# Performance work log

Hardware: AMD Instinct MI355X
Metric: run time of the kernel (lower is better)

## Reference

```python
import jax, jax.numpy as jnp
import numpy as np

B, T, C, H = 4, 4096, 1024, 128

def setup_inputs() -> dict:
    key = jax.random.key(0)
    kx, kq, kk, kv = jax.random.split(key, 4)
    s = 1.0 / np.sqrt(C)
    return {
        "x": jax.random.normal(kx, (B, T, C), dtype=jnp.float32),
        "Wq": jax.random.normal(kq, (C, H), dtype=jnp.float32) * s,
        "Wk": jax.random.normal(kk, (C, H), dtype=jnp.float32) * s,
        "Wv": jax.random.normal(kv, (C, H), dtype=jnp.float32) * s,
    }

def reference(x, Wq, Wk, Wv):
    # x: [B,T,C]; projections to [B,T,H]
    q = jnp.einsum('btc,ch->bth', x, Wq)
    k = jnp.einsum('btc,ch->bth', x, Wk)
    v = jnp.einsum('btc,ch->bth', x, Wv)
    scale = 1.0 / jnp.sqrt(jnp.asarray(H, dtype=x.dtype))
    wei = jnp.einsum('bqh,bkh->bqk', q, k) * scale  # [B,T,T]
    causal = jnp.tril(jnp.ones((T, T), dtype=bool))
    wei = jnp.where(causal, wei, -jnp.inf)
    wei = jax.nn.softmax(wei, axis=-1)
    # dropout p=0.0 -> identity
    out = jnp.einsum('bqk,bkh->bqh', wei, v)
    return out
```

## Files before the change

### kernel.cpp

```cpp
#include <hip/hip_runtime.h>
#include <hip/hip_bf16.h>

#define B_ 4
#define T_ 4096
#define C_ 1024
#define H_ 128
#define SEG_ 8

typedef __attribute__((ext_vector_type(8))) short short8;
typedef __attribute__((ext_vector_type(4))) float f32x4;
typedef __attribute__((ext_vector_type(4))) unsigned short u16x4;

static __device__ __forceinline__ unsigned short f2bf(float f) {
    union { float f; unsigned u; } v; v.f = f;
    unsigned r = v.u + 0x7FFF + ((v.u >> 16) & 1);
    return (unsigned short)(r >> 16);
}

__global__ void wt_kernel(const float* __restrict__ Wq, const float* __restrict__ Wk,
                          const float* __restrict__ Wv, unsigned short* __restrict__ Wt) {
    __shared__ float tile[64][65];
    int c0 = blockIdx.x * 64, h0 = blockIdx.y * 64, w = blockIdx.z;
    const float* W = (w == 0) ? Wq : (w == 1) ? Wk : Wv;
    unsigned short* dst = Wt + (size_t)w * H_ * C_;
    int tr = threadIdx.x >> 6, tc = threadIdx.x & 63;
#pragma unroll
    for (int p = 0; p < 16; ++p) {
        int r = p * 4 + tr;
        tile[r][tc] = W[(size_t)(c0 + r) * H_ + h0 + tc];
    }
    __syncthreads();
#pragma unroll
    for (int p = 0; p < 16; ++p) {
        int r = p * 4 + tr;
        dst[(size_t)(h0 + r) * C_ + c0 + tc] = f2bf(tile[tc][r]);
    }
}

__global__ __launch_bounds__(256) void proj_kernel(
        const float* __restrict__ x, const unsigned short* __restrict__ Wt3,
        unsigned short* __restrict__ Q, unsigned short* __restrict__ K,
        unsigned short* __restrict__ Vt) {
    __shared__ unsigned short Xs[32 * 64];
    int m0 = blockIdx.x * 32;
    int tid = threadIdx.x;
    int lane = tid & 63, wid = tid >> 6;
    int l15 = lane & 15, g = lane >> 4;
    int l7 = l15 & 7;

    f32x4 acc[2][6];
#pragma unroll
    for (int i = 0; i < 2; i++)
#pragma unroll
        for (int j = 0; j < 6; j++) acc[i][j] = (f32x4)0.0f;

    for (int kt = 0; kt < C_ / 64; ++kt) {
        int k0 = kt * 64;
        {
            int r = tid >> 3, c8 = tid & 7;
            const float* src = x + (size_t)(m0 + r) * C_ + k0 + c8 * 8;
            float4 v0 = *(const float4*)src;
            float4 v1 = *(const float4*)(src + 4);
            union { short8 s; u16x4 h[2]; } pk;
            pk.h[0].x = f2bf(v0.x); pk.h[0].y = f2bf(v0.y);
            pk.h[0].z = f2bf(v0.z); pk.h[0].w = f2bf(v0.w);
            pk.h[1].x = f2bf(v1.x); pk.h[1].y = f2bf(v1.y);
            pk.h[1].z = f2bf(v1.z); pk.h[1].w = f2bf(v1.w);
            *(short8*)&Xs[r * 64 + ((c8 ^ (r & 7)) << 3)] = pk.s;
        }
        __syncthreads();
#pragma unroll
        for (int kf = 0; kf < 2; ++kf) {
            short8 a[2], bv[6];
#pragma unroll
            for (int mt = 0; mt < 2; mt++) {
                int row = mt * 16 + l15;
                a[mt] = *(const short8*)&Xs[row * 64 + (((kf * 4 + g) ^ l7) << 3)];
            }
#pragma unroll
            for (int nt = 0; nt < 6; nt++) {
                int r = wid * 96 + nt * 16 + l15;
                bv[nt] = *(const short8*)(Wt3 + (size_t)r * C_ + k0 + (kf * 4 + g) * 8);
            }
#pragma unroll
            for (int mt = 0; mt < 2; mt++)
#pragma unroll
                for (int nt = 0; nt < 6; nt++)
                    acc[mt][nt] = __builtin_amdgcn_mfma_f32_16x16x32_bf16(a[mt], bv[nt], acc[mt][nt], 0, 0, 0);
        }
        __syncthreads();
    }
    int b = m0 >> 12;
    int tbase = m0 & (T_ - 1);
#pragma unroll
    for (int nt = 0; nt < 6; nt++) {
        int col = wid * 96 + nt * 16 + l15;
        int w = col >> 7, h = col & 127;
#pragma unroll
        for (int mt = 0; mt < 2; mt++) {
            if (w < 2) {
                unsigned short* outp = (w == 0) ? Q : K;
                int row0 = m0 + mt * 16 + g * 4;
#pragma unroll
                for (int ri = 0; ri < 4; ri++)
                    outp[(size_t)(row0 + ri) * H_ + h] = f2bf(acc[mt][nt][ri]);
            } else {
                int t0 = tbase + mt * 16 + g * 4;
                u16x4 o;
                o.x = f2bf(acc[mt][nt][0]); o.y = f2bf(acc[mt][nt][1]);
                o.z = f2bf(acc[mt][nt][2]); o.w = f2bf(acc[mt][nt][3]);
                *(u16x4*)&Vt[(size_t)(b * H_ + h) * T_ + t0] = o;
            }
        }
    }
}

__global__ __launch_bounds__(256) void attn_kernel(
        const unsigned short* __restrict__ Q, const unsigned short* __restrict__ K,
        const unsigned short* __restrict__ Vt,
        float* __restrict__ Opart, float* __restrict__ Lpart) {
    int qb = blockIdx.x, seg = blockIdx.y, b = blockIdx.z;
    if (seg * SEG_ > qb) return;
    __shared__ unsigned short KsF[64 * 128];
    __shared__ unsigned short VsF[128 * 64];
    __shared__ unsigned short PsF[4][16 * 64];
    int tid = threadIdx.x, lane = tid & 63, wid = tid >> 6;
    int l15 = lane & 15, g = lane >> 4;
    int l7 = l15 & 7;
    int q0w = qb * 64 + wid * 16;
    const float alpha = 0.08838834764831845f;

    short8 aq[4];
#pragma unroll
    for (int kf = 0; kf < 4; kf++)
        aq[kf] = *(const short8*)(Q + (size_t)(b * T_ + q0w + l15) * H_ + kf * 32 + g * 8);

    f32x4 o[8];
#pragma unroll
    for (int i = 0; i < 8; i++) o[i] = (f32x4)0.0f;
    float l_run[4];
#pragma unroll
    for (int ri = 0; ri < 4; ri++) l_run[ri] = 0.f;

    int kt0 = seg * SEG_;
    int kt_end = min(qb, kt0 + SEG_ - 1);

    short8 kreg[4], vreg[4];
#define LOAD_KV(KT) do { int k0_ = (KT) * 64; \
    _Pragma("unroll") \
    for (int p = 0; p < 4; ++p) { int idx = tid + p * 256; \
        kreg[p] = *(const short8*)(K + (size_t)(b * T_ + k0_ + (idx >> 4)) * H_ + (idx & 15) * 8); } \
    _Pragma("unroll") \
    for (int p = 0; p < 4; ++p) { int idx = tid + p * 256; \
        vreg[p] = *(const short8*)(Vt + (size_t)(b * H_ + (idx >> 3)) * T_ + k0_ + (idx & 7) * 8); } \
    } while (0)

    LOAD_KV(kt0);
    for (int kt = kt0; kt <= kt_end; ++kt) {
        int k0 = kt * 64;
        __syncthreads();
#pragma unroll
        for (int p = 0; p < 4; ++p) {
            int idx = tid + p * 256;
            int r = idx >> 4;
            *(short8*)&KsF[r * 128 + (((idx & 15) ^ (r & 7)) << 3)] = kreg[p];
        }
#pragma unroll
        for (int p = 0; p < 4; ++p) {
            int idx = tid + p * 256;
            int r = idx >> 3;
            *(short8*)&VsF[r * 64 + (((idx & 7) ^ (r & 7)) << 3)] = vreg[p];
        }
        __syncthreads();
        if (kt < kt_end) LOAD_KV(kt + 1);

        f32x4 s[4];
#pragma unroll
        for (int ct = 0; ct < 4; ct++) {
            s[ct] = (f32x4)0.0f;
#pragma unroll
            for (int kf = 0; kf < 4; kf++) {
                int row = ct * 16 + l15;
                short8 bk = *(const short8*)&KsF[row * 128 + (((kf * 4 + g) ^ l7) << 3)];
                s[ct] = __builtin_amdgcn_mfma_f32_16x16x32_bf16(aq[kf], bk, s[ct], 0, 0, 0);
            }
        }
        bool diag = (kt == qb);
#pragma unroll
        for (int ct = 0; ct < 4; ct++)
#pragma unroll
            for (int ri = 0; ri < 4; ri++) {
                float v = s[ct][ri] * alpha;
                if (diag) {
                    int kkg = k0 + ct * 16 + l15;
                    int qg = q0w + g * 4 + ri;
                    if (kkg > qg) v = -1e30f;
                }
                float p = __expf(v);
                l_run[ri] += p;
                int row = g * 4 + ri;
                PsF[wid][row * 64 + (((2 * ct + (l15 >> 3)) ^ (row & 7)) << 3) + l7] = f2bf(p);
            }

#pragma unroll
        for (int kf2 = 0; kf2 < 2; kf2++) {
            short8 ap = *(const short8*)&PsF[wid][l15 * 64 + (((kf2 * 4 + g) ^ l7) << 3)];
#pragma unroll
            for (int ht = 0; ht < 8; ht++) {
                int row = ht * 16 + l15;
                short8 bv = *(const short8*)&VsF[row * 64 + (((kf2 * 4 + g) ^ l7) << 3)];
                o[ht] = __builtin_amdgcn_mfma_f32_16x16x32_bf16(ap, bv, o[ht], 0, 0, 0);
            }
        }
    }
#undef LOAD_KV

    size_t slot = (((size_t)b * (T_ / 64) + qb) * 8 + seg);
    float* Ob = Opart + slot * 64 * 128;
    float* Lb = Lpart + slot * 64;
#pragma unroll
    for (int ri = 0; ri < 4; ri++) {
        float l = l_run[ri];
#pragma unroll
        for (int off = 1; off < 16; off <<= 1)
            l += __shfl_xor(l, off, 64);
        int qrow = wid * 16 + g * 4 + ri;
        Lb[qrow] = l;
#pragma unroll
        for (int ht = 0; ht < 8; ht++)
            Ob[(size_t)qrow * 128 + ht * 16 + l15] = o[ht][ri];
    }
}

__global__ __launch_bounds__(256) void combine_kernel(
        const float* __restrict__ Opart, const float* __restrict__ Lpart,
        float* __restrict__ out) {
    int qt = blockIdx.x, b = blockIdx.y;
    int nseg = qt / SEG_ + 1;
    int tid = threadIdx.x;
    size_t obase = (((size_t)b * (T_ / 64) + qt) * 8) * 64 * 128;
    size_t lbase = (((size_t)b * (T_ / 64) + qt) * 8) * 64;
    float4* dst = (float4*)(out + ((size_t)b * T_ + qt * 64) * 128);
#pragma unroll
    for (int i = 0; i < 8; ++i) {
        int e4 = tid + i * 256;
        int q = e4 >> 5;
        float4 acc = {0.f, 0.f, 0.f, 0.f};
        float lsum = 0.f;
        for (int s = 0; s < nseg; ++s) {
            float4 v = *((const float4*)(Opart + obase + (size_t)s * 64 * 128) + e4);
            acc.x += v.x; acc.y += v.y; acc.z += v.z; acc.w += v.w;
            lsum += Lpart[lbase + s * 64 + q];
        }
        float inv = 1.0f / lsum;
        float4 r = {acc.x * inv, acc.y * inv, acc.z * inv, acc.w * inv};
        dst[e4] = r;
    }
}

extern "C" void kernel_launch(void* const* d_in, const int* in_sizes, int n_in,
                              void* d_out, int out_size, void* d_ws, size_t ws_size,
                              hipStream_t stream) {
    const float* x  = (const float*)d_in[0];
    const float* Wq = (const float*)d_in[1];
    const float* Wk = (const float*)d_in[2];
    const float* Wv = (const float*)d_in[3];
    float* out = (float*)d_out;

    unsigned short* Wt = (unsigned short*)d_ws;
    unsigned short* Qb = Wt + 3 * (size_t)H_ * C_;
    unsigned short* Kb = Qb + (size_t)B_ * T_ * H_;
    unsigned short* Vt = Kb + (size_t)B_ * T_ * H_;
    float* Opart = (float*)(Vt + (size_t)B_ * T_ * H_);
    float* Lpart = Opart + (size_t)B_ * 64 * 8 * 64 * 128;

    wt_kernel<<<dim3(C_ / 64, H_ / 64, 3), 256, 0, stream>>>(Wq, Wk, Wv, Wt);
    proj_kernel<<<dim3((B_ * T_) / 32), 256, 0, stream>>>(x, Wt, Qb, Kb, Vt);
    attn_kernel<<<dim3(T_ / 64, 8, B_), 256, 0, stream>>>(Qb, Kb, Vt, Opart, Lpart);
    combine_kernel<<<dim3(T_ / 64, B_), 256, 0, stream>>>(Opart, Lpart, out);
}
```

Baseline: 215.7 us.

## Stage weights in LDS with double-buffered 64-row projection tiles; split combine blocks

```diff
diff --git a/kernel.cpp b/kernel.cpp
--- a/kernel.cpp
+++ b/kernel.cpp
@@ -37,75 +37,104 @@
     }
 }
 
-__global__ __launch_bounds__(256) void proj_kernel(
+__global__ __launch_bounds__(256, 1) void proj_kernel(
         const float* __restrict__ x, const unsigned short* __restrict__ Wt3,
         unsigned short* __restrict__ Q, unsigned short* __restrict__ K,
         unsigned short* __restrict__ Vt) {
-    __shared__ unsigned short Xs[32 * 64];
-    int m0 = blockIdx.x * 32;
+    __shared__ unsigned short Xs[2][64 * 64];
+    __shared__ unsigned short Wsh[2][384 * 64];
+    int m0 = blockIdx.x * 64;
     int tid = threadIdx.x;
     int lane = tid & 63, wid = tid >> 6;
+    int mw = wid >> 1, nw = wid & 1;
     int l15 = lane & 15, g = lane >> 4;
     int l7 = l15 & 7;
 
-    f32x4 acc[2][6];
+    f32x4 acc[2][12];
 #pragma unroll
     for (int i = 0; i < 2; i++)
 #pragma unroll
-        for (int j = 0; j < 6; j++) acc[i][j] = (f32x4)0.0f;
-
-    for (int kt = 0; kt < C_ / 64; ++kt) {
-        int k0 = kt * 64;
-        {
-            int r = tid >> 3, c8 = tid & 7;
-            const float* src = x + (size_t)(m0 + r) * C_ + k0 + c8 * 8;
-            float4 v0 = *(const float4*)src;
-            float4 v1 = *(const float4*)(src + 4);
-            union { short8 s; u16x4 h[2]; } pk;
-            pk.h[0].x = f2bf(v0.x); pk.h[0].y = f2bf(v0.y);
-            pk.h[0].z = f2bf(v0.z); pk.h[0].w = f2bf(v0.w);
-            pk.h[1].x = f2bf(v1.x); pk.h[1].y = f2bf(v1.y);
-            pk.h[1].z = f2bf(v1.z); pk.h[1].w = f2bf(v1.w);
-            *(short8*)&Xs[r * 64 + ((c8 ^ (r & 7)) << 3)] = pk.s;
-        }
+        for (int j = 0; j < 12; j++) acc[i][j] = (f32x4)0.0f;
+
+    float4 xreg[2][2];
+    short8 wreg[12];
+
+#define PROJ_LOAD(KT) do { int k0_ = (KT) * 64; \
+    _Pragma("unroll") \
+    for (int p = 0; p < 2; ++p) { \
+        int idx = tid + p * 256; int r = idx >> 3, cg = idx & 7; \
+        const float* src = x + (size_t)(m0 + r) * C_ + k0_ + cg * 8; \
+        xreg[p][0] = *(const float4*)src; xreg[p][1] = *(const float4*)(src + 4); } \
+    _Pragma("unroll") \
+    for (int p = 0; p < 12; ++p) { \
+        int idx = tid + p * 256; int r = idx >> 3, cg = idx & 7; \
+        wreg[p] = *(const short8*)(Wt3 + (size_t)r * C_ + k0_ + cg * 8); } \
+    } while (0)
+
+#define PROJ_WRITE(BUF) do { \
+    _Pragma("unroll") \
+    for (int p = 0; p < 2; ++p) { \
+        int idx = tid + p * 256; int r = idx >> 3, cg = idx & 7; \
+        union { short8 s; u16x4 h[2]; } pk; \
+        pk.h[0].x = f2bf(xreg[p][0].x); pk.h[0].y = f2bf(xreg[p][0].y); \
+        pk.h[0].z = f2bf(xreg[p][0].z); pk.h[0].w = f2bf(xreg[p][0].w); \
+        pk.h[1].x = f2bf(xreg[p][1].x); pk.h[1].y = f2bf(xreg[p][1].y); \
+        pk.h[1].z = f2bf(xreg[p][1].z); pk.h[1].w = f2bf(xreg[p][1].w); \
+        *(short8*)&Xs[BUF][r * 64 + ((cg ^ (r & 7)) << 3)] = pk.s; } \
+    _Pragma("unroll") \
+    for (int p = 0; p < 12; ++p) { \
+        int idx = tid + p * 256; int r = idx >> 3, cg = idx & 7; \
+        *(short8*)&Wsh[BUF][r * 64 + ((cg ^ (r & 7)) << 3)] = wreg[p]; } \
+    } while (0)
+
+    PROJ_LOAD(0);
+    PROJ_WRITE(0);
+    __syncthreads();
+
+    for (int kt = 0; kt < 16; ++kt) {
+        int cur = kt & 1;
+        if (kt < 15) PROJ_LOAD(kt + 1);
+#pragma unroll
+        for (int kf = 0; kf < 2; ++kf) {
+            short8 a[2], bv[12];
+#pragma unroll
+            for (int mt = 0; mt < 2; mt++) {
+                int row = mw * 32 + mt * 16 + l15;
+                a[mt] = *(const short8*)&Xs[cur][row * 64 + (((kf * 4 + g) ^ (row & 7)) << 3)];
+            }
+#pragma unroll
+            for (int nt = 0; nt < 12; nt++) {
+                int row = nw * 192 + nt * 16 + l15;
+                bv[nt] = *(const short8*)&Wsh[cur][row * 64 + (((kf * 4 + g) ^ (row & 7)) << 3)];
+            }
+#pragma unroll
+            for (int mt = 0; mt < 2; mt++)
+#pragma unroll
+                for (int nt = 0; nt < 12; nt++)
+                    acc[mt][nt] = __builtin_amdgcn_mfma_f32_16x16x32_bf16(a[mt], bv[nt], acc[mt][nt], 0, 0, 0);
+        }
+        if (kt < 15) PROJ_WRITE(cur ^ 1);
         __syncthreads();
-#pragma unroll
-        for (int kf = 0; kf < 2; ++kf) {
-            short8 a[2], bv[6];
-#pragma unroll
-            for (int mt = 0; mt < 2; mt++) {
-                int row = mt * 16 + l15;
-                a[mt] = *(const short8*)&Xs[row * 64 + (((kf * 4 + g) ^ l7) << 3)];
-            }
-#pragma unroll
-            for (int nt = 0; nt < 6; nt++) {
-                int r = wid * 96 + nt * 16 + l15;
-                bv[nt] = *(const short8*)(Wt3 + (size_t)r * C_ + k0 + (kf * 4 + g) * 8);
-            }
-#pragma unroll
-            for (int mt = 0; mt < 2; mt++)
-#pragma unroll
-                for (int nt = 0; nt < 6; nt++)
-                    acc[mt][nt] = __builtin_amdgcn_mfma_f32_16x16x32_bf16(a[mt], bv[nt], acc[mt][nt], 0, 0, 0);
-        }
-        __syncthreads();
-    }
+    }
+#undef PROJ_LOAD
+#undef PROJ_WRITE
+
     int b = m0 >> 12;
     int tbase = m0 & (T_ - 1);
 #pragma unroll
-    for (int nt = 0; nt < 6; nt++) {
-        int col = wid * 96 + nt * 16 + l15;
+    for (int nt = 0; nt < 12; nt++) {
+        int col = nw * 192 + nt * 16 + l15;
         int w = col >> 7, h = col & 127;
 #pragma unroll
         for (int mt = 0; mt < 2; mt++) {
             if (w < 2) {
                 unsigned short* outp = (w == 0) ? Q : K;
-                int row0 = m0 + mt * 16 + g * 4;
+                int row0 = m0 + mw * 32 + mt * 16 + g * 4;
 #pragma unroll
                 for (int ri = 0; ri < 4; ri++)
                     outp[(size_t)(row0 + ri) * H_ + h] = f2bf(acc[mt][nt][ri]);
             } else {
-                int t0 = tbase + mt * 16 + g * 4;
+                int t0 = tbase + mw * 32 + mt * 16 + g * 4;
                 u16x4 o;
                 o.x = f2bf(acc[mt][nt][0]); o.y = f2bf(acc[mt][nt][1]);
                 o.z = f2bf(acc[mt][nt][2]); o.w = f2bf(acc[mt][nt][3]);
@@ -235,14 +264,14 @@
 __global__ __launch_bounds__(256) void combine_kernel(
         const float* __restrict__ Opart, const float* __restrict__ Lpart,
         float* __restrict__ out) {
-    int qt = blockIdx.x, b = blockIdx.y;
+    int qt = blockIdx.x, b = blockIdx.y, half = blockIdx.z;
     int nseg = qt / SEG_ + 1;
     int tid = threadIdx.x;
-    size_t obase = (((size_t)b * (T_ / 64) + qt) * 8) * 64 * 128;
-    size_t lbase = (((size_t)b * (T_ / 64) + qt) * 8) * 64;
-    float4* dst = (float4*)(out + ((size_t)b * T_ + qt * 64) * 128);
-#pragma unroll
-    for (int i = 0; i < 8; ++i) {
+    size_t obase = (((size_t)b * (T_ / 64) + qt) * 8) * 64 * 128 + (size_t)half * 32 * 128;
+    size_t lbase = (((size_t)b * (T_ / 64) + qt) * 8) * 64 + half * 32;
+    float4* dst = (float4*)(out + ((size_t)b * T_ + qt * 64 + half * 32) * 128);
+#pragma unroll
+    for (int i = 0; i < 4; ++i) {
         int e4 = tid + i * 256;
         int q = e4 >> 5;
         float4 acc = {0.f, 0.f, 0.f, 0.f};
@@ -275,7 +304,7 @@
     float* Lpart = Opart + (size_t)B_ * 64 * 8 * 64 * 128;
 
     wt_kernel<<<dim3(C_ / 64, H_ / 64, 3), 256, 0, stream>>>(Wq, Wk, Wv, Wt);
-    proj_kernel<<<dim3((B_ * T_) / 32), 256, 0, stream>>>(x, Wt, Qb, Kb, Vt);
+    proj_kernel<<<dim3((B_ * T_) / 64), 256, 0, stream>>>(x, Wt, Qb, Kb, Vt);
     attn_kernel<<<dim3(T_ / 64, 8, B_), 256, 0, stream>>>(Qb, Kb, Vt, Opart, Lpart);
-    combine_kernel<<<dim3(T_ / 64, B_), 256, 0, stream>>>(Opart, Lpart, out);
-}
+    combine_kernel<<<dim3(T_ / 64, B_, 2), 256, 0, stream>>>(Opart, Lpart, out);
+}
```

Result: faster. 186.0 us (-13.7%).
